# Kernel tuning notes

Hardware: AMD Instinct MI355X
Metric: run time of the kernel (lower is better)

Reference implementation:

```python
import jax, jax.numpy as jnp
import numpy as np

A = 32          # num input capsule types
PSIZE = 16      # caps_size (pose matrix 4x4)
MD = 4          # mat_dim = sqrt(caps_size)
NCLS = 10       # output capsules / classes
KF = 5          # routing kernel (final_shape)
KK = KF * KF
KKA = KK * A
ITERS = 3
FINAL_LAMBDA = 0.01
EPS = 1e-12
LN2PI = float(np.log(2.0 * np.pi))
BN_EPS = 1e-5


def unfold(x, k, stride, pad):
    # torch.nn.functional.unfold: [b,C,h,w] -> [b, C*k*k, L], (c, kh, kw) channel-major
    b, c, h, w = x.shape
    if pad:
        x = jnp.pad(x, ((0, 0), (0, 0), (pad, pad), (pad, pad)))
    oh = (h + 2 * pad - k) // stride + 1
    ow = (w + 2 * pad - k) // stride + 1
    cols = jnp.stack([
        jnp.stack([x[:, :, i:i + stride * oh:stride, j:j + stride * ow:stride]
                   for j in range(k)], axis=3)
        for i in range(k)], axis=2)          # [b, c, k, k, oh, ow]
    return cols.reshape(b, c * k * k, oh * ow)


def conv3x3(x, w):
    return jax.lax.conv_general_dilated(x, w, (1, 1), [(1, 1), (1, 1)],
                                        dimension_numbers=('NCHW', 'OIHW', 'NCHW'))


def bn_inf(x, g, b, m, v):
    scale = g / jnp.sqrt(v + BN_EPS)
    return (x - m[None, :, None, None]) * scale[None, :, None, None] + b[None, :, None, None]


def em_routing(a_in, pose, W, beta_u, beta_a):
    b = a_in.shape[0]
    # pose votes
    pu = unfold(pose, KF, 1, 0)                     # [b, A*PSIZE*KK, l]
    l = pu.shape[-1]
    pu = pu.reshape(b, A, PSIZE, KK, l).transpose(0, 4, 3, 1, 2).reshape(b, l, KKA, PSIZE)
    pm = pu.reshape(b, l, KKA, MD, MD)[:, :, :, None]        # [b,l,kkA,1,md,md]
    v = jnp.matmul(pm, W)                                    # [b,l,kkA,B,md,md]
    v = v.reshape(b, l, KKA, NCLS, PSIZE)
    # activations
    au = unfold(a_in, KF, 1, 0).reshape(b, A, KK, l).transpose(0, 3, 2, 1).reshape(b, l, KKA)
    r = jnp.ones((b, l, KKA, NCLS, 1), v.dtype)
    a_out = mu = None
    for i in range(ITERS):
        lam = FINAL_LAMBDA * (1.0 - 0.95 ** (i + 1))
        # M-step
        rw = r * au[:, :, :, None, None]
        r_sum = rw.sum(axis=2, keepdims=True)                # [b,l,1,B,1]
        coeff = rw / (r_sum + EPS)
        mu = (coeff * v).sum(axis=2, keepdims=True)          # [b,l,1,B,psize]
        sigma_sq = (coeff * (v - mu) ** 2).sum(axis=2, keepdims=True) + EPS
        r_s = r_sum[:, :, 0]                                 # [b,l,B,1]
        sig = sigma_sq[:, :, 0]                              # [b,l,B,psize]
        cost_h = (beta_u + 0.5 * jnp.log(sig)) * r_s         # log(sqrt(s)) = 0.5*log(s)
        a_out = jax.nn.sigmoid(lam * (beta_a - cost_h.sum(axis=3)))   # [b,l,B]
        if i < ITERS - 1:
            # E-step (note: log(sigma_sq * ln2pi) as in original code)
            ln_p = (-0.5 * jnp.sum(jnp.log(sigma_sq * LN2PI), axis=-1)
                    - jnp.sum((v - mu) ** 2 / (2.0 * sigma_sq), axis=-1))   # [b,l,kkA,B]
            ln_ap = ln_p + jnp.log(a_out)[:, :, None, :]
            r = jax.nn.softmax(ln_ap, axis=-1)[..., None]
    oh = int(np.floor(np.sqrt(l)))
    pose_out = mu[:, :, 0].reshape(b, l, -1).transpose(0, 2, 1).reshape(b, -1, oh, oh)
    a_map = a_out.transpose(0, 2, 1).reshape(b, -1, oh, oh)
    return a_map, pose_out


def setup_inputs():
    key = jax.random.key(0)
    ks = jax.random.split(key, 14)
    batch = 256
    x = jax.random.normal(ks[0], (batch, 512, 5, 5), jnp.float32)
    w_a = jax.random.normal(ks[1], (A, 512, 3, 3), jnp.float32) * 0.02
    w_pose = jax.random.normal(ks[2], (A * PSIZE, 512, 3, 3), jnp.float32) * 0.02
    bn_a_g = 1.0 + 0.1 * jax.random.normal(ks[3], (A,), jnp.float32)
    bn_a_b = 0.1 * jax.random.normal(ks[4], (A,), jnp.float32)
    bn_a_m = 0.1 * jax.random.normal(ks[5], (A,), jnp.float32)
    bn_a_v = jax.random.uniform(ks[6], (A,), jnp.float32, 0.5, 1.5)
    C2 = A * PSIZE
    bn_p_g = 1.0 + 0.1 * jax.random.normal(ks[7], (C2,), jnp.float32)
    bn_p_b = 0.1 * jax.random.normal(ks[8], (C2,), jnp.float32)
    bn_p_m = 0.1 * jax.random.normal(ks[9], (C2,), jnp.float32)
    bn_p_v = jax.random.uniform(ks[10], (C2,), jnp.float32, 0.5, 1.5)
    W = jax.random.normal(ks[11], (KKA, NCLS, MD, MD), jnp.float32) * 0.25
    beta_u = jnp.zeros((1, 1, NCLS, 1), jnp.float32)
    beta_a = jnp.zeros((1, 1, NCLS), jnp.float32)
    return {"x": x, "w_a": w_a, "w_pose": w_pose,
            "bn_a_g": bn_a_g, "bn_a_b": bn_a_b, "bn_a_m": bn_a_m, "bn_a_v": bn_a_v,
            "bn_p_g": bn_p_g, "bn_p_b": bn_p_b, "bn_p_m": bn_p_m, "bn_p_v": bn_p_v,
            "W": W, "beta_u": beta_u, "beta_a": beta_a}


def reference(x, w_a, w_pose, bn_a_g, bn_a_b, bn_a_m, bn_a_v,
              bn_p_g, bn_p_b, bn_p_m, bn_p_v, W, beta_u, beta_a):
    a = jax.nn.sigmoid(bn_inf(conv3x3(x, w_a), bn_a_g, bn_a_b, bn_a_m, bn_a_v))
    pose = bn_inf(conv3x3(x, w_pose), bn_p_g, bn_p_b, bn_p_m, bn_p_v)
    a_map, _ = em_routing(a, pose, W, beta_u, beta_a)
    out = a_map.reshape(a_map.shape[0], -1)          # [b, 10]
    out = out / out.sum(axis=1, keepdims=True)
    return jnp.log(out)
```

## Files before the change

kernel.cpp:

```cpp
#include <hip/hip_runtime.h>
#include <math.h>

#define CIN 512
#define NCLS 10
#define KDIM 4608
#define NTOT 6400
#define MPAD 640
#define BK 128
#define NKT 36
#define NABLK (5 * NKT)
#define LN2PI_F 1.8378770664093453f

typedef __attribute__((ext_vector_type(8))) short bf16x8;
typedef __attribute__((ext_vector_type(4))) float f32x4;

typedef const __attribute__((address_space(1))) void* gas_ptr;
typedef __attribute__((address_space(3))) void* las_ptr;

__device__ __forceinline__ void async_copy16(const void* g, void* l) {
    __builtin_amdgcn_global_load_lds((gas_ptr)g, (las_ptr)l, 16, 0, 0);
}

__device__ __forceinline__ unsigned short f2bf(float f) {
    unsigned int u = __float_as_uint(f);
    u = (u + 0x7fffu + ((u >> 16) & 1u)) >> 16;
    return (unsigned short)u;
}
__device__ __forceinline__ float bf2f(unsigned short s) {
    return __uint_as_float(((unsigned int)s) << 16);
}
__device__ __forceinline__ float fexp(float x) { return __expf(x); }
__device__ __forceinline__ float flog(float x) { return __logf(x); }

__global__ __launch_bounds__(1024) void pack_kernel(
    const float* __restrict__ x,
    const float* __restrict__ w_pose, const float* __restrict__ w_a,
    const float* __restrict__ bn_p_g, const float* __restrict__ bn_p_b,
    const float* __restrict__ bn_p_m, const float* __restrict__ bn_p_v,
    const float* __restrict__ bn_a_g, const float* __restrict__ bn_a_b,
    const float* __restrict__ bn_a_m, const float* __restrict__ bn_a_v,
    const float* __restrict__ Wm,
    unsigned short* __restrict__ At, unsigned short* __restrict__ Wmb,
    float* __restrict__ sc, float* __restrict__ bi,
    unsigned short* __restrict__ Bt)
{
    __shared__ __align__(16) float xs[CIN * 25];
    const int bid = blockIdx.x;
    const int t = threadIdx.x;

    if (bid < 256) {
        const int b = bid;
        const float4* xb = reinterpret_cast<const float4*>(x + (size_t)b * (CIN * 25));
        for (int f4 = t; f4 < (CIN * 25) / 4; f4 += 1024)
            reinterpret_cast<float4*>(xs)[f4] = xb[f4];
        __syncthreads();

        for (int w = t; w < 25 * (KDIM / 8); w += 1024) {
            const int ch = w / 25;
            const int px = w - ch * 25;
            const int py = px / 5, qx = px % 5;
            const int k0 = ch * 8;
            unsigned short v[8];
            #pragma unroll
            for (int j = 0; j < 8; ++j) {
                const int k = k0 + j;
                const int ci = k / 9;
                const int kk = k - ci * 9;
                const int dy = kk / 3, dx = kk - dy * 3;
                const int yy = py + dy - 1, xx = qx + dx - 1;
                const bool ok = (yy >= 0) & (yy < 5) & (xx >= 0) & (xx < 5);
                v[j] = ok ? f2bf(xs[ci * 25 + yy * 5 + xx]) : (unsigned short)0;
            }
            int4 o;
            o.x = (int)v[0] | ((int)v[1] << 16);
            o.y = (int)v[2] | ((int)v[3] << 16);
            o.z = (int)v[4] | ((int)v[5] << 16);
            o.w = (int)v[6] | ((int)v[7] << 16);
            const int n = b * 25 + px;
            const int nblk = n >> 7, nr = n & 127;
            const int kt = k0 >> 7;
            const int kc8 = (k0 >> 3) & 15;
            const int c = kc8 * 128 + (nr ^ (kc8 << 2));
            reinterpret_cast<int4*>(Bt + ((((size_t)(nblk * NKT + kt)) << 11) + c) * 8)[0] = o;
        }
        return;
    }

    const int f = (bid - 256) * 1024 + t;
    const int vblk = f >> 8, vt = f & 255;
    if (vblk >= NABLK + 63) return;

    if (vblk >= NABLK) {
        const int chunk = (vblk - NABLK) * 256 + vt;
        if (chunk < 16000) {
            const int e = chunk >> 1, half = chunk & 1;
            const int m = e / 10, c = e - m * 10;
            const int kk = m >> 5, a = m & 31;
            const int de = (kk * 10 + c) * 32 + a;
            const float4* s4 = reinterpret_cast<const float4*>(Wm + (size_t)chunk * 8);
            float4 x0 = s4[0], x1 = s4[1];
            int4 o;
            o.x = (int)f2bf(x0.x) | ((int)f2bf(x0.y) << 16);
            o.y = (int)f2bf(x0.z) | ((int)f2bf(x0.w) << 16);
            o.z = (int)f2bf(x1.x) | ((int)f2bf(x1.y) << 16);
            o.w = (int)f2bf(x1.z) | ((int)f2bf(x1.w) << 16);
            reinterpret_cast<int4*>(Wmb + ((size_t)de * 2 + half) * 8)[0] = o;
        }
        return;
    }

    const int mblk = vblk / NKT;
    if (vblk == 0) {
        for (int i = vt; i < MPAD; i += 256) {
            float s = 0.f, b = 0.f;
            if (i < 512) {
                s = bn_p_g[i] / sqrtf(bn_p_v[i] + 1e-5f);
                b = bn_p_b[i] - bn_p_m[i] * s;
            } else if (i < 544) {
                const int j = i - 512;
                s = bn_a_g[j] / sqrtf(bn_a_v[j] + 1e-5f);
                b = bn_a_b[j] - bn_a_m[j] * s;
            }
            sc[i] = s; bi[i] = b;
        }
    }

    const int kt = vblk - mblk * NKT;
    #pragma unroll
    for (int j = 0; j < 8; ++j) {
        const int c = vt + j * 256;
        const int kc8 = c >> 7, slot = c & 127;
        const int row = mblk * 128 + (slot ^ (kc8 << 2));
        const int k0 = (kt * 16 + kc8) * 8;
        float v[8] = {0.f,0.f,0.f,0.f,0.f,0.f,0.f,0.f};
        if (row < 512) {
            const float4* s4 = reinterpret_cast<const float4*>(w_pose + (size_t)row * KDIM + k0);
            float4 x0 = s4[0], x1 = s4[1];
            v[0]=x0.x; v[1]=x0.y; v[2]=x0.z; v[3]=x0.w;
            v[4]=x1.x; v[5]=x1.y; v[6]=x1.z; v[7]=x1.w;
        } else if (row < 544) {
            const float4* s4 = reinterpret_cast<const float4*>(w_a + (size_t)(row - 512) * KDIM + k0);
            float4 x0 = s4[0], x1 = s4[1];
            v[0]=x0.x; v[1]=x0.y; v[2]=x0.z; v[3]=x0.w;
            v[4]=x1.x; v[5]=x1.y; v[6]=x1.z; v[7]=x1.w;
        }
        int4 o;
        o.x = (int)f2bf(v[0]) | ((int)f2bf(v[1]) << 16);
        o.y = (int)f2bf(v[2]) | ((int)f2bf(v[3]) << 16);
        o.z = (int)f2bf(v[4]) | ((int)f2bf(v[5]) << 16);
        o.w = (int)f2bf(v[6]) | ((int)f2bf(v[7]) << 16);
        reinterpret_cast<int4*>(At + ((((size_t)vblk) << 11) + c) * 8)[0] = o;
    }
}

__global__ __launch_bounds__(1024) void gemm_kernel(
    const unsigned short* __restrict__ At,
    const unsigned short* __restrict__ Bt,
    const float* __restrict__ sc, const float* __restrict__ bi,
    unsigned short* __restrict__ Cp,
    float* __restrict__ Ca)
{
    __shared__ __align__(16) unsigned char smem[131072];
    const int t = threadIdx.x;
    const int L = blockIdx.x;
    int mblk, nblk;
    if (L >= 240) { const int i = L - 240; mblk = i >> 1; nblk = 48 + (i & 1); }
    else          { const int q = L / 40, r = L - q * 40;
                    mblk = r >> 3; nblk = q * 8 + (r & 7); }
    const int m0 = mblk * 128, n0 = nblk * 128;
    const int lane = t & 63, w = t >> 6;
    const int g = w >> 2, wq = w & 3;
    const int wm = wq >> 1, wn = wq & 1;
    const int row16 = lane & 15, quad = lane >> 4;

    f32x4 acc[4][4] = {};

    const unsigned short* gAbase = At + (((size_t)mblk * NKT) << 14);
    const unsigned short* gBbase = Bt + (((size_t)nblk * NKT) << 14);

    #define STAGE(kt, s)                                                      \
    {                                                                         \
        unsigned short* As_ = (unsigned short*)(smem + (s) * 65536);          \
        unsigned short* Bs_ = As_ + 16384;                                    \
        const unsigned short* ga = gAbase + ((size_t)(kt) << 14);             \
        const unsigned short* gb = gBbase + ((size_t)(kt) << 14);             \
        _Pragma("unroll")                                                     \
        for (int j = 0; j < 2; ++j) {                                         \
            async_copy16(ga + ((size_t)(j * 1024 + t) << 3),                  \
                         As_ + ((size_t)(j * 1024 + w * 64) << 3));           \
            async_copy16(gb + ((size_t)(j * 1024 + t) << 3),                  \
                         Bs_ + ((size_t)(j * 1024 + w * 64) << 3));           \
        }                                                                     \
    }

    #define COMPUTE(s)                                                        \
    {                                                                         \
        const unsigned short* As_ = (const unsigned short*)(smem + (s) * 65536);\
        const unsigned short* Bs_ = As_ + 16384;                              \
        const int kc8b = g * 4 + quad;                                        \
        const int sw = kc8b << 2;                                             \
        bf16x8 af[4], bfr[4];                                                 \
        _Pragma("unroll")                                                     \
        for (int mt = 0; mt < 4; ++mt)                                        \
            af[mt] = *reinterpret_cast<const bf16x8*>(                        \
                &As_[(size_t)(kc8b * 128 + ((wm * 64 + mt * 16 + row16) ^ sw)) * 8]);\
        _Pragma("unroll")                                                     \
        for (int nt = 0; nt < 4; ++nt)                                        \
            bfr[nt] = *reinterpret_cast<const bf16x8*>(                       \
                &Bs_[(size_t)(kc8b * 128 + ((wn * 64 + nt * 16 + row16) ^ sw)) * 8]);\
        _Pragma("unroll")                                                     \
        for (int mt = 0; mt < 4; ++mt)                                        \
            _Pragma("unroll")                                                 \
            for (int nt = 0; nt < 4; ++nt)                                    \
                acc[mt][nt] = __builtin_amdgcn_mfma_f32_16x16x32_bf16(        \
                    af[mt], bfr[nt], acc[mt][nt], 0, 0, 0);                   \
    }

    STAGE(0, 0);
    for (int kt = 0; kt < NKT; ++kt) {
        __syncthreads();
        if (kt + 1 < NKT) STAGE(kt + 1, (kt + 1) & 1);
        COMPUTE(kt & 1);
    }
    #undef STAGE
    #undef COMPUTE

    f32x4* mb = (f32x4*)smem;
    #pragma unroll
    for (int r = 1; r < 4; ++r) {
        __syncthreads();
        if (g == r) {
            f32x4* dst = mb + wq * 1024;
            #pragma unroll
            for (int i = 0; i < 16; ++i)
                dst[i * 64 + lane] = acc[i >> 2][i & 3];
        }
        __syncthreads();
        if (g == 0) {
            const f32x4* src = mb + wq * 1024;
            #pragma unroll
            for (int i = 0; i < 16; ++i)
                acc[i >> 2][i & 3] += src[i * 64 + lane];
        }
    }

    if (g == 0) {
        #pragma unroll
        for (int mt = 0; mt < 4; ++mt) {
            const int mbase = m0 + wm * 64 + mt * 16 + quad * 4;
            if (mbase >= 544) continue;
            #pragma unroll
            for (int rg = 0; rg < 4; ++rg) {
                const int m = mbase + rg;
                const float s = sc[m], bbx = bi[m];
                #pragma unroll
                for (int nt = 0; nt < 4; ++nt) {
                    const int n = n0 + wn * 64 + nt * 16 + row16;
                    const float v = fmaf(acc[mt][nt][rg], s, bbx);
                    if (m < 512) Cp[(size_t)m * NTOT + n] = f2bf(v);
                    else Ca[(size_t)(m - 512) * NTOT + n] = 1.f / (1.f + fexp(-v));
                }
            }
        }
    }
}

__global__ __launch_bounds__(640, 1) void em_kernel(
    const unsigned short* __restrict__ Cp,
    const float* __restrict__ Ca,
    const unsigned short* __restrict__ Wmb,
    const float* __restrict__ beta_u, const float* __restrict__ beta_a,
    float* __restrict__ out)
{
    __shared__ __align__(16) unsigned short psh[25][2][32][8];
    __shared__ __align__(16) unsigned short wsh[2 * 20480];
    __shared__ float aush[800];
    __shared__ float lnq[NCLS][800];
    __shared__ float mu_sh[NCLS][16];
    __shared__ float i2s_sh[NCLS][16];
    __shared__ float costp[2][NCLS];
    __shared__ float slgp[2][NCLS];
    __shared__ float Kc_sh[NCLS];
    __shared__ float aout_sh[NCLS];

    const int b = blockIdx.x, t = threadIdx.x;
    const int c = t >> 6;
    const int rh = (t >> 5) & 1;
    const int a = t & 31;

    const int gu = t ^ ((t >> 3) & 3);
    const int r2 = (c * 32 + a) * 2;
    const int u0 = r2 ^ ((r2 >> 3) & 3);

    #define STAGEW(qq, ss)                                                   \
    {                                                                        \
        const int nkk_ = ((qq) == 6) ? 1 : 4;                                \
        const unsigned short* gW = Wmb + (size_t)(qq) * 4 * 5120;            \
        unsigned short* lW = wsh + (size_t)(ss) * 20480;                     \
        for (int kki = 0; kki < nkk_; ++kki)                                 \
            async_copy16(gW + (size_t)(kki * 640 + gu) * 8,                  \
                         lW + (size_t)(kki * 640 + t) * 8);                  \
    }

    const unsigned short* pb = Cp + (size_t)b * 25;
    for (int f = t; f < 12800; f += 640) {
        const int c2 = f / 25, px = f - c2 * 25;
        const int e = c2 & 15;
        psh[px][e >> 3][c2 >> 4][e & 7] = pb[(size_t)c2 * NTOT + px];
    }
    const float* ab = Ca + (size_t)b * 25;
    for (int f = t; f < 800; f += 640) {
        const int ci = f / 25, px = f - ci * 25;
        aush[px * 32 + ci] = ab[(size_t)ci * NTOT + px];
    }
    __syncthreads();

    const float bu = beta_u[c], ba = beta_a[c];
    float muL[8], i2sL[8], KcL = 0.f;

    #define VOTE(w0_, w1_, p_, vv)                                           \
        {                                                                    \
            float pm[8], wv[16];                                             \
            const unsigned int pu[4] = {(unsigned)p_.x, (unsigned)p_.y,      \
                                        (unsigned)p_.z, (unsigned)p_.w};     \
            _Pragma("unroll")                                                \
            for (int i = 0; i < 4; ++i) {                                    \
                pm[2*i]   = __uint_as_float(pu[i] << 16);                    \
                pm[2*i+1] = __uint_as_float(pu[i] & 0xFFFF0000u);            \
            }                                                                \
            const unsigned int uu[8] = {(unsigned)w0_.x,(unsigned)w0_.y,     \
                (unsigned)w0_.z,(unsigned)w0_.w,(unsigned)w1_.x,             \
                (unsigned)w1_.y,(unsigned)w1_.z,(unsigned)w1_.w};            \
            _Pragma("unroll")                                                \
            for (int i = 0; i < 8; ++i) {                                    \
                wv[2*i]   = __uint_as_float(uu[i] << 16);                    \
                wv[2*i+1] = __uint_as_float(uu[i] & 0xFFFF0000u);            \
            }                                                                \
            _Pragma("unroll")                                                \
            for (int jr = 0; jr < 2; ++jr) {                                 \
                _Pragma("unroll")                                            \
                for (int s = 0; s < 4; ++s) {                                \
                    float av = 0.f;                                          \
                    _Pragma("unroll")                                        \
                    for (int tt = 0; tt < 4; ++tt)                           \
                        av = fmaf(pm[jr*4+tt], wv[tt*4+s], av);              \
                    vv[jr*4+s] = av;                                         \
                }                                                            \
            }                                                                \
        }

    float p95 = 1.f;
    for (int it = 0; it < 3; ++it) {
        p95 *= 0.95f;
        const float lam = 0.01f * (1.f - p95);

        if (it > 0) {
            STAGEW(0, 0);
            __syncthreads();
            for (int qc = 0; qc < 7; ++qc) {
                if (qc < 6) STAGEW(qc + 1, (qc + 1) & 1);
                const unsigned short* wb = wsh + (size_t)(qc & 1) * 20480;
                #pragma unroll
                for (int kkin = 0; kkin < 4; ++kkin) {
                    const int kk = qc * 4 + kkin;
                    if (kk < 25) {
                        const unsigned short* wrow = wb + kkin * 5120;
                        const int4 w0 = *reinterpret_cast<const int4*>(wrow + (size_t)u0 * 8);
                        const int4 w1 = *reinterpret_cast<const int4*>(wrow + (size_t)(u0 ^ 1) * 8);
                        const int4 p = *reinterpret_cast<const int4*>(&psh[kk][rh][a][0]);
                        float vv[8];
                        VOTE(w0, w1, p, vv);
                        float qacc = (rh == 0) ? KcL : 0.f;
                        #pragma unroll
                        for (int j = 0; j < 8; ++j) {
                            const float d = vv[j] - muL[j];
                            qacc -= d * d * i2sL[j];
                        }
                        qacc += __shfl_xor(qacc, 32);
                        if (rh == 0) lnq[c][kk * 32 + a] = qacc;
                    }
                }
                __syncthreads();
            }
            for (int m = t; m < 800; m += 640) {
                float qv[NCLS];
                #pragma unroll
                for (int cc = 0; cc < NCLS; ++cc) qv[cc] = lnq[cc][m];
                float mx = qv[0];
                #pragma unroll
                for (int cc = 1; cc < NCLS; ++cc) mx = fmaxf(mx, qv[cc]);
                float ev[NCLS];
                float den = 0.f;
                #pragma unroll
                for (int cc = 0; cc < NCLS; ++cc) {
                    ev[cc] = fexp(qv[cc] - mx);
                    den += ev[cc];
                }
                const float s = aush[m] * __builtin_amdgcn_rcpf(den);
                #pragma unroll
                for (int cc = 0; cc < NCLS; ++cc)
                    lnq[cc][m] = ev[cc] * s;
            }
            __syncthreads();
        }

        float S0 = 0.f, S1[8], S2[8];
        #pragma unroll
        for (int j = 0; j < 8; ++j) { S1[j] = 0.f; S2[j] = 0.f; }

        STAGEW(0, 0);
        __syncthreads();
        for (int qc = 0; qc < 7; ++qc) {
            if (qc < 6) STAGEW(qc + 1, (qc + 1) & 1);
            const unsigned short* wb = wsh + (size_t)(qc & 1) * 20480;
            #pragma unroll
            for (int kkin = 0; kkin < 4; ++kkin) {
                const int kk = qc * 4 + kkin;
                if (kk < 25) {
                    const unsigned short* wrow = wb + kkin * 5120;
                    const int4 w0 = *reinterpret_cast<const int4*>(wrow + (size_t)u0 * 8);
                    const int4 w1 = *reinterpret_cast<const int4*>(wrow + (size_t)(u0 ^ 1) * 8);
                    const int4 p = *reinterpret_cast<const int4*>(&psh[kk][rh][a][0]);
                    float vv[8];
                    VOTE(w0, w1, p, vv);
                    const int m = kk * 32 + a;
                    const float rw = (it == 0) ? aush[m] : lnq[c][m];
                    S0 += rw;
                    #pragma unroll
                    for (int j = 0; j < 8; ++j) {
                        const float rv = rw * vv[j];
                        S1[j] += rv;
                        S2[j] = fmaf(rv, vv[j], S2[j]);
                    }
                }
            }
            __syncthreads();
        }

        #pragma unroll
        for (int off = 16; off >= 1; off >>= 1) {
            S0 += __shfl_xor(S0, off);
            #pragma unroll
            for (int j = 0; j < 8; ++j) {
                S1[j] += __shfl_xor(S1[j], off);
                S2[j] += __shfl_xor(S2[j], off);
            }
        }

        if (a == 0) {
            const float s0e = S0 + 1e-12f;
            const float inv = 1.f / s0e;
            float cost_ = 0.f, slg_ = 0.f;
            #pragma unroll
            for (int j = 0; j < 8; ++j) {
                const float mu_ = S1[j] * inv;
                const float sg = (S2[j] - 2.f * mu_ * S1[j] + mu_ * mu_ * S0) * inv
                                 + 1e-12f;
                cost_ += bu + 0.5f * flog(sg);
                slg_ += flog(sg * LN2PI_F);
                mu_sh[c][rh * 8 + j] = mu_;
                i2s_sh[c][rh * 8 + j] = 0.5f / sg;
            }
            costp[rh][c] = cost_;
            slgp[rh][c] = slg_;
        }
        __syncthreads();
        if (a == 0 && rh == 0) {
            const float costsum = (costp[0][c] + costp[1][c]) * S0;
            const float aout = 1.f / (1.f + fexp(-(lam * (ba - costsum))));
            aout_sh[c] = aout;
            Kc_sh[c] = flog(aout) - 0.5f * (slgp[0][c] + slgp[1][c]);
        }
        __syncthreads();
        if (it < 2) {
            #pragma unroll
            for (int j = 0; j < 8; ++j) {
                muL[j] = mu_sh[c][rh * 8 + j];
                i2sL[j] = i2s_sh[c][rh * 8 + j];
            }
            KcL = Kc_sh[c];
        }
    }

    if (t < NCLS) {
        float s = 0.f;
        #pragma unroll
        for (int cc = 0; cc < NCLS; ++cc) s += aout_sh[cc];
        out[b * NCLS + t] = flog(aout_sh[t] / s);
    }
    #undef VOTE
    #undef STAGEW
}

extern "C" void kernel_launch(void* const* d_in, const int* in_sizes, int n_in,
                              void* d_out, int out_size, void* d_ws, size_t ws_size,
                              hipStream_t stream) {
    const float* x      = (const float*)d_in[0];
    const float* w_a    = (const float*)d_in[1];
    const float* w_pose = (const float*)d_in[2];
    const float* bn_a_g = (const float*)d_in[3];
    const float* bn_a_b = (const float*)d_in[4];
    const float* bn_a_m = (const float*)d_in[5];
    const float* bn_a_v = (const float*)d_in[6];
    const float* bn_p_g = (const float*)d_in[7];
    const float* bn_p_b = (const float*)d_in[8];
    const float* bn_p_m = (const float*)d_in[9];
    const float* bn_p_v = (const float*)d_in[10];
    const float* Wm     = (const float*)d_in[11];
    const float* beta_u = (const float*)d_in[12];
    const float* beta_a = (const float*)d_in[13];
    float* out = (float*)d_out;

    char* p = (char*)d_ws;
    unsigned short* At  = (unsigned short*)p;  p += (size_t)MPAD * KDIM * 2;
    unsigned short* Bt  = (unsigned short*)p;  p += (size_t)NTOT * KDIM * 2;
    unsigned short* Wmb = (unsigned short*)p;  p += (size_t)800 * NCLS * 16 * 2;
    unsigned short* Cp  = (unsigned short*)p;  p += (size_t)512 * NTOT * 2;
    float* Ca = (float*)p;                     p += (size_t)32 * NTOT * 4;
    float* sc = (float*)p;                     p += MPAD * 4;
    float* bi = (float*)p;                     p += MPAD * 4;

    pack_kernel<<<317, 1024, 0, stream>>>(x, w_pose, w_a,
                                          bn_p_g, bn_p_b, bn_p_m, bn_p_v,
                                          bn_a_g, bn_a_b, bn_a_m, bn_a_v,
                                          Wm, At, Wmb, sc, bi, Bt);
    gemm_kernel<<<250, 1024, 0, stream>>>(At, Bt, sc, bi, Cp, Ca);
    em_kernel<<<256, 640, 0, stream>>>(Cp, Ca, Wmb, beta_u, beta_a, out);
}
```

Baseline: 230.9 us.

## Load routing weights directly from global into registers, drop LDS staging

The EM routing kernel no longer double-buffers the transformation weights W through shared memory with async copies and per-chunk barriers. Each thread now reads its own 32-byte weight slice straight from global memory into registers, prefetching one step ahead. The 25 kernel positions are split into two interleaved streams (0-12 and 13-24) with separate accumulators to raise instruction-level parallelism. This removes seven block-wide syncs per pass and frees 80 KB of LDS, but relies on L2/cache hits for the repeated per-block weight reads and uses more registers.

New measurement: 233.1 us. No clear change (+1.0%).

```diff
diff --git a/kernel.cpp b/kernel.cpp
--- a/kernel.cpp
+++ b/kernel.cpp
@@ -273,7 +273,6 @@
     float* __restrict__ out)
 {
     __shared__ __align__(16) unsigned short psh[25][2][32][8];
-    __shared__ __align__(16) unsigned short wsh[2 * 20480];
     __shared__ float aush[800];
     __shared__ float lnq[NCLS][800];
     __shared__ float mu_sh[NCLS][16];
@@ -288,20 +287,6 @@
     const int rh = (t >> 5) & 1;
     const int a = t & 31;
 
-    const int gu = t ^ ((t >> 3) & 3);
-    const int r2 = (c * 32 + a) * 2;
-    const int u0 = r2 ^ ((r2 >> 3) & 3);
-
-    #define STAGEW(qq, ss)                                                   \
-    {                                                                        \
-        const int nkk_ = ((qq) == 6) ? 1 : 4;                                \
-        const unsigned short* gW = Wmb + (size_t)(qq) * 4 * 5120;            \
-        unsigned short* lW = wsh + (size_t)(ss) * 20480;                     \
-        for (int kki = 0; kki < nkk_; ++kki)                                 \
-            async_copy16(gW + (size_t)(kki * 640 + gu) * 8,                  \
-                         lW + (size_t)(kki * 640 + t) * 8);                  \
-    }
-
     const unsigned short* pb = Cp + (size_t)b * 25;
     for (int f = t; f < 12800; f += 640) {
         const int c2 = f / 25, px = f - c2 * 25;
@@ -317,6 +302,8 @@
 
     const float bu = beta_u[c], ba = beta_a[c];
     float muL[8], i2sL[8], KcL = 0.f;
+    const unsigned short* wbase  = Wmb + ((size_t)(c * 32 + a)) * 16;
+    const unsigned short* wbaseB = wbase + (size_t)13 * 5120;
 
     #define VOTE(w0_, w1_, p_, vv)                                           \
         {                                                                    \
@@ -355,33 +342,53 @@
         const float lam = 0.01f * (1.f - p95);
 
         if (it > 0) {
-            STAGEW(0, 0);
+            int4 wA0 = *reinterpret_cast<const int4*>(wbase);
+            int4 wA1 = *reinterpret_cast<const int4*>(wbase + 8);
+            int4 wB0 = *reinterpret_cast<const int4*>(wbaseB);
+            int4 wB1 = *reinterpret_cast<const int4*>(wbaseB + 8);
+            int4 pA = *reinterpret_cast<const int4*>(&psh[0][rh][a][0]);
+            int4 pB = *reinterpret_cast<const int4*>(&psh[13][rh][a][0]);
+            for (int kh = 0; kh < 13; ++kh) {
+                const int4 a0 = wA0, a1 = wA1, p0 = pA;
+                const int4 b0 = wB0, b1 = wB1, p1 = pB;
+                if (kh < 12) {
+                    const unsigned short* wnA = wbase + (size_t)(kh + 1) * 5120;
+                    wA0 = *reinterpret_cast<const int4*>(wnA);
+                    wA1 = *reinterpret_cast<const int4*>(wnA + 8);
+                    pA  = *reinterpret_cast<const int4*>(&psh[kh + 1][rh][a][0]);
+                    if (kh < 11) {
+                        const unsigned short* wnB = wbaseB + (size_t)(kh + 1) * 5120;
+                        wB0 = *reinterpret_cast<const int4*>(wnB);
+                        wB1 = *reinterpret_cast<const int4*>(wnB + 8);
+                        pB  = *reinterpret_cast<const int4*>(&psh[kh + 14][rh][a][0]);
+                    }
+                }
+                float vvA[8];
+                VOTE(a0, a1, p0, vvA);
+                float qA = (rh == 0) ? KcL : 0.f;
+                #pragma unroll
+                for (int j = 0; j < 8; ++j) {
+                    const float d = vvA[j] - muL[j];
+                    qA -= d * d * i2sL[j];
+                }
+                float qB = (rh == 0) ? KcL : 0.f;
+                if (kh < 12) {
+                    float vvB[8];
+                    VOTE(b0, b1, p1, vvB);
+                    #pragma unroll
+                    for (int j = 0; j < 8; ++j) {
+                        const float d = vvB[j] - muL[j];
+                        qB -= d * d * i2sL[j];
+                    }
+                }
+                qA += __shfl_xor(qA, 32);
+                qB += __shfl_xor(qB, 32);
+                if (rh == 0) {
+                    lnq[c][kh * 32 + a] = qA;
+                    if (kh < 12) lnq[c][(kh + 13) * 32 + a] = qB;
+                }
+            }
             __syncthreads();
-            for (int qc = 0; qc < 7; ++qc) {
-                if (qc < 6) STAGEW(qc + 1, (qc + 1) & 1);
-                const unsigned short* wb = wsh + (size_t)(qc & 1) * 20480;
-                #pragma unroll
-                for (int kkin = 0; kkin < 4; ++kkin) {
-                    const int kk = qc * 4 + kkin;
-                    if (kk < 25) {
-                        const unsigned short* wrow = wb + kkin * 5120;
-                        const int4 w0 = *reinterpret_cast<const int4*>(wrow + (size_t)u0 * 8);
-                        const int4 w1 = *reinterpret_cast<const int4*>(wrow + (size_t)(u0 ^ 1) * 8);
-                        const int4 p = *reinterpret_cast<const int4*>(&psh[kk][rh][a][0]);
-                        float vv[8];
-                        VOTE(w0, w1, p, vv);
-                        float qacc = (rh == 0) ? KcL : 0.f;
-                        #pragma unroll
-                        for (int j = 0; j < 8; ++j) {
-                            const float d = vv[j] - muL[j];
-                            qacc -= d * d * i2sL[j];
-                        }
-                        qacc += __shfl_xor(qacc, 32);
-                        if (rh == 0) lnq[c][kk * 32 + a] = qacc;
-                    }
-                }
-                __syncthreads();
-            }
             for (int m = t; m < 800; m += 640) {
                 float qv[NCLS];
                 #pragma unroll
@@ -404,39 +411,65 @@
             __syncthreads();
         }
 
-        float S0 = 0.f, S1[8], S2[8];
+        float S0a = 0.f, S1a[8], S2a[8];
+        float S0b = 0.f, S1b[8], S2b[8];
         #pragma unroll
-        for (int j = 0; j < 8; ++j) { S1[j] = 0.f; S2[j] = 0.f; }
-
-        STAGEW(0, 0);
-        __syncthreads();
-        for (int qc = 0; qc < 7; ++qc) {
-            if (qc < 6) STAGEW(qc + 1, (qc + 1) & 1);
-            const unsigned short* wb = wsh + (size_t)(qc & 1) * 20480;
-            #pragma unroll
-            for (int kkin = 0; kkin < 4; ++kkin) {
-                const int kk = qc * 4 + kkin;
-                if (kk < 25) {
-                    const unsigned short* wrow = wb + kkin * 5120;
-                    const int4 w0 = *reinterpret_cast<const int4*>(wrow + (size_t)u0 * 8);
-                    const int4 w1 = *reinterpret_cast<const int4*>(wrow + (size_t)(u0 ^ 1) * 8);
-                    const int4 p = *reinterpret_cast<const int4*>(&psh[kk][rh][a][0]);
-                    float vv[8];
-                    VOTE(w0, w1, p, vv);
-                    const int m = kk * 32 + a;
-                    const float rw = (it == 0) ? aush[m] : lnq[c][m];
-                    S0 += rw;
-                    #pragma unroll
-                    for (int j = 0; j < 8; ++j) {
-                        const float rv = rw * vv[j];
-                        S1[j] += rv;
-                        S2[j] = fmaf(rv, vv[j], S2[j]);
-                    }
-                }
-            }
-            __syncthreads();
-        }
-
+        for (int j = 0; j < 8; ++j) { S1a[j] = 0.f; S2a[j] = 0.f;
+                                      S1b[j] = 0.f; S2b[j] = 0.f; }
+
+        int4 wA0 = *reinterpret_cast<const int4*>(wbase);
+        int4 wA1 = *reinterpret_cast<const int4*>(wbase + 8);
+        int4 wB0 = *reinterpret_cast<const int4*>(wbaseB);
+        int4 wB1 = *reinterpret_cast<const int4*>(wbaseB + 8);
+        int4 pA = *reinterpret_cast<const int4*>(&psh[0][rh][a][0]);
+        int4 pB = *reinterpret_cast<const int4*>(&psh[13][rh][a][0]);
+        for (int kh = 0; kh < 13; ++kh) {
+            const int4 a0 = wA0, a1 = wA1, p0 = pA;
+            const int4 b0 = wB0, b1 = wB1, p1 = pB;
+            if (kh < 12) {
+                const unsigned short* wnA = wbase + (size_t)(kh + 1) * 5120;
+                wA0 = *reinterpret_cast<const int4*>(wnA);
+                wA1 = *reinterpret_cast<const int4*>(wnA + 8);
+                pA  = *reinterpret_cast<const int4*>(&psh[kh + 1][rh][a][0]);
+                if (kh < 11) {
+                    const unsigned short* wnB = wbaseB + (size_t)(kh + 1) * 5120;
+                    wB0 = *reinterpret_cast<const int4*>(wnB);
+                    wB1 = *reinterpret_cast<const int4*>(wnB + 8);
+                    pB  = *reinterpret_cast<const int4*>(&psh[kh + 14][rh][a][0]);
+                }
+            }
+            {
+                float vvA[8];
+                VOTE(a0, a1, p0, vvA);
+                const int m = kh * 32 + a;
+                const float rw = (it == 0) ? aush[m] : lnq[c][m];
+                S0a += rw;
+                #pragma unroll
+                for (int j = 0; j < 8; ++j) {
+                    const float rv = rw * vvA[j];
+                    S1a[j] += rv;
+                    S2a[j] = fmaf(rv, vvA[j], S2a[j]);
+                }
+            }
+            if (kh < 12) {
+                float vvB[8];
+                VOTE(b0, b1, p1, vvB);
+                const int m = (kh + 13) * 32 + a;
+                const float rw = (it == 0) ? aush[m] : lnq[c][m];
+                S0b += rw;
+                #pragma unroll
+                for (int j = 0; j < 8; ++j) {
+                    const float rv = rw * vvB[j];
+                    S1b[j] += rv;
+                    S2b[j] = fmaf(rv, vvB[j], S2b[j]);
+                }
+            }
+        }
+
+        float S0 = S0a + S0b, S1[8], S2[8];
+        #pragma unroll
+        for (int j = 0; j < 8; ++j) { S1[j] = S1a[j] + S1b[j];
+                                      S2[j] = S2a[j] + S2b[j]; }
         #pragma unroll
         for (int off = 16; off >= 1; off >>= 1) {
             S0 += __shfl_xor(S0, off);
@@ -489,7 +522,6 @@
         out[b * NCLS + t] = flog(aout_sh[t] / s);
     }
     #undef VOTE
-    #undef STAGEW
 }
 
 extern "C" void kernel_launch(void* const* d_in, const int* in_sizes, int n_in,
```

## Read fp32 routing weights directly from global with register prefetch instead of LDS staging

Applied to the files above, without the earlier changes.

The EM routing kernel no longer stages bf16 transform weights into double-buffered shared memory with async copies and per-chunk barriers. Each thread now loads its own fp32 weight rows straight from global memory (L2-resident, shared across the 256 blocks) with one- or two-step register prefetch. This removes the barriers and the bf16 unpacking inside the vote loops and raises weight precision to fp32. In exchange it doubles weight bytes and relies on cache hits for the repeated per-block reads.

After: 405.2 us. 1.75x slower.

```diff
diff --git a/kernel.cpp b/kernel.cpp
--- a/kernel.cpp
+++ b/kernel.cpp
@@ -40,7 +40,7 @@
     const float* __restrict__ bn_a_g, const float* __restrict__ bn_a_b,
     const float* __restrict__ bn_a_m, const float* __restrict__ bn_a_v,
     const float* __restrict__ Wm,
-    unsigned short* __restrict__ At, unsigned short* __restrict__ Wmb,
+    unsigned short* __restrict__ At, float* __restrict__ Wmbf,
     float* __restrict__ sc, float* __restrict__ bi,
     unsigned short* __restrict__ Bt)
 {
@@ -98,13 +98,9 @@
             const int kk = m >> 5, a = m & 31;
             const int de = (kk * 10 + c) * 32 + a;
             const float4* s4 = reinterpret_cast<const float4*>(Wm + (size_t)chunk * 8);
-            float4 x0 = s4[0], x1 = s4[1];
-            int4 o;
-            o.x = (int)f2bf(x0.x) | ((int)f2bf(x0.y) << 16);
-            o.y = (int)f2bf(x0.z) | ((int)f2bf(x0.w) << 16);
-            o.z = (int)f2bf(x1.x) | ((int)f2bf(x1.y) << 16);
-            o.w = (int)f2bf(x1.z) | ((int)f2bf(x1.w) << 16);
-            reinterpret_cast<int4*>(Wmb + ((size_t)de * 2 + half) * 8)[0] = o;
+            float4* d4 = reinterpret_cast<float4*>(Wmbf + ((size_t)de * 2 + half) * 8);
+            d4[0] = s4[0];
+            d4[1] = s4[1];
         }
         return;
     }
@@ -268,12 +264,11 @@
 __global__ __launch_bounds__(640, 1) void em_kernel(
     const unsigned short* __restrict__ Cp,
     const float* __restrict__ Ca,
-    const unsigned short* __restrict__ Wmb,
+    const float* __restrict__ Wmbf,
     const float* __restrict__ beta_u, const float* __restrict__ beta_a,
     float* __restrict__ out)
 {
     __shared__ __align__(16) unsigned short psh[25][2][32][8];
-    __shared__ __align__(16) unsigned short wsh[2 * 20480];
     __shared__ float aush[800];
     __shared__ float lnq[NCLS][800];
     __shared__ float mu_sh[NCLS][16];
@@ -288,20 +283,6 @@
     const int rh = (t >> 5) & 1;
     const int a = t & 31;
 
-    const int gu = t ^ ((t >> 3) & 3);
-    const int r2 = (c * 32 + a) * 2;
-    const int u0 = r2 ^ ((r2 >> 3) & 3);
-
-    #define STAGEW(qq, ss)                                                   \
-    {                                                                        \
-        const int nkk_ = ((qq) == 6) ? 1 : 4;                                \
-        const unsigned short* gW = Wmb + (size_t)(qq) * 4 * 5120;            \
-        unsigned short* lW = wsh + (size_t)(ss) * 20480;                     \
-        for (int kki = 0; kki < nkk_; ++kki)                                 \
-            async_copy16(gW + (size_t)(kki * 640 + gu) * 8,                  \
-                         lW + (size_t)(kki * 640 + t) * 8);                  \
-    }
-
     const unsigned short* pb = Cp + (size_t)b * 25;
     for (int f = t; f < 12800; f += 640) {
         const int c2 = f / 25, px = f - c2 * 25;
@@ -317,10 +298,11 @@
 
     const float bu = beta_u[c], ba = beta_a[c];
     float muL[8], i2sL[8], KcL = 0.f;
-
-    #define VOTE(w0_, w1_, p_, vv)                                           \
+    const float* wbase = Wmbf + ((size_t)(c * 32 + a)) * 16;
+
+    #define VOTE(w0_, w1_, w2_, w3_, p_, vv)                                 \
         {                                                                    \
-            float pm[8], wv[16];                                             \
+            float pm[8];                                                     \
             const unsigned int pu[4] = {(unsigned)p_.x, (unsigned)p_.y,      \
                                         (unsigned)p_.z, (unsigned)p_.w};     \
             _Pragma("unroll")                                                \
@@ -328,14 +310,10 @@
                 pm[2*i]   = __uint_as_float(pu[i] << 16);                    \
                 pm[2*i+1] = __uint_as_float(pu[i] & 0xFFFF0000u);            \
             }                                                                \
-            const unsigned int uu[8] = {(unsigned)w0_.x,(unsigned)w0_.y,     \
-                (unsigned)w0_.z,(unsigned)w0_.w,(unsigned)w1_.x,             \
-                (unsigned)w1_.y,(unsigned)w1_.z,(unsigned)w1_.w};            \
-            _Pragma("unroll")                                                \
-            for (int i = 0; i < 8; ++i) {                                    \
-                wv[2*i]   = __uint_as_float(uu[i] << 16);                    \
-                wv[2*i+1] = __uint_as_float(uu[i] & 0xFFFF0000u);            \
-            }                                                                \
+            const float wv[16] = {w0_.x, w0_.y, w0_.z, w0_.w,                \
+                                  w1_.x, w1_.y, w1_.z, w1_.w,                \
+                                  w2_.x, w2_.y, w2_.z, w2_.w,                \
+                                  w3_.x, w3_.y, w3_.z, w3_.w};               \
             _Pragma("unroll")                                                \
             for (int jr = 0; jr < 2; ++jr) {                                 \
                 _Pragma("unroll")                                            \
@@ -355,33 +333,30 @@
         const float lam = 0.01f * (1.f - p95);
 
         if (it > 0) {
-            STAGEW(0, 0);
+            const float4* wp = reinterpret_cast<const float4*>(wbase);
+            float4 r0 = wp[0], r1 = wp[1], r2 = wp[2], r3 = wp[3];
+            int4 pr = *reinterpret_cast<const int4*>(&psh[0][rh][a][0]);
+            for (int kk = 0; kk < 25; ++kk) {
+                const float4 w0 = r0, w1 = r1, w2 = r2, w3 = r3;
+                const int4 p = pr;
+                if (kk < 24) {
+                    const float4* wn = reinterpret_cast<const float4*>(
+                        wbase + (size_t)(kk + 1) * 5120);
+                    r0 = wn[0]; r1 = wn[1]; r2 = wn[2]; r3 = wn[3];
+                    pr = *reinterpret_cast<const int4*>(&psh[kk + 1][rh][a][0]);
+                }
+                float vv[8];
+                VOTE(w0, w1, w2, w3, p, vv);
+                float q = (rh == 0) ? KcL : 0.f;
+                #pragma unroll
+                for (int j = 0; j < 8; ++j) {
+                    const float d = vv[j] - muL[j];
+                    q -= d * d * i2sL[j];
+                }
+                q += __shfl_xor(q, 32);
+                if (rh == 0) lnq[c][kk * 32 + a] = q;
+            }
             __syncthreads();
-            for (int qc = 0; qc < 7; ++qc) {
-                if (qc < 6) STAGEW(qc + 1, (qc + 1) & 1);
-                const unsigned short* wb = wsh + (size_t)(qc & 1) * 20480;
-                #pragma unroll
-                for (int kkin = 0; kkin < 4; ++kkin) {
-                    const int kk = qc * 4 + kkin;
-                    if (kk < 25) {
-                        const unsigned short* wrow = wb + kkin * 5120;
-                        const int4 w0 = *reinterpret_cast<const int4*>(wrow + (size_t)u0 * 8);
-                        const int4 w1 = *reinterpret_cast<const int4*>(wrow + (size_t)(u0 ^ 1) * 8);
-                        const int4 p = *reinterpret_cast<const int4*>(&psh[kk][rh][a][0]);
-                        float vv[8];
-                        VOTE(w0, w1, p, vv);
-                        float qacc = (rh == 0) ? KcL : 0.f;
-                        #pragma unroll
-                        for (int j = 0; j < 8; ++j) {
-                            const float d = vv[j] - muL[j];
-                            qacc -= d * d * i2sL[j];
-                        }
-                        qacc += __shfl_xor(qacc, 32);
-                        if (rh == 0) lnq[c][kk * 32 + a] = qacc;
-                    }
-                }
-                __syncthreads();
-            }
             for (int m = t; m < 800; m += 640) {
                 float qv[NCLS];
                 #pragma unroll
@@ -408,33 +383,33 @@
         #pragma unroll
         for (int j = 0; j < 8; ++j) { S1[j] = 0.f; S2[j] = 0.f; }
 
-        STAGEW(0, 0);
-        __syncthreads();
-        for (int qc = 0; qc < 7; ++qc) {
-            if (qc < 6) STAGEW(qc + 1, (qc + 1) & 1);
-            const unsigned short* wb = wsh + (size_t)(qc & 1) * 20480;
-            #pragma unroll
-            for (int kkin = 0; kkin < 4; ++kkin) {
-                const int kk = qc * 4 + kkin;
-                if (kk < 25) {
-                    const unsigned short* wrow = wb + kkin * 5120;
-                    const int4 w0 = *reinterpret_cast<const int4*>(wrow + (size_t)u0 * 8);
-                    const int4 w1 = *reinterpret_cast<const int4*>(wrow + (size_t)(u0 ^ 1) * 8);
-                    const int4 p = *reinterpret_cast<const int4*>(&psh[kk][rh][a][0]);
-                    float vv[8];
-                    VOTE(w0, w1, p, vv);
-                    const int m = kk * 32 + a;
-                    const float rw = (it == 0) ? aush[m] : lnq[c][m];
-                    S0 += rw;
-                    #pragma unroll
-                    for (int j = 0; j < 8; ++j) {
-                        const float rv = rw * vv[j];
-                        S1[j] += rv;
-                        S2[j] = fmaf(rv, vv[j], S2[j]);
-                    }
-                }
-            }
-            __syncthreads();
+        const float4* wpA = reinterpret_cast<const float4*>(wbase);
+        const float4* wpB = reinterpret_cast<const float4*>(wbase + 5120);
+        float4 a0 = wpA[0], a1 = wpA[1], a2 = wpA[2], a3 = wpA[3];
+        float4 b0 = wpB[0], b1 = wpB[1], b2 = wpB[2], b3 = wpB[3];
+        int4 pr = *reinterpret_cast<const int4*>(&psh[0][rh][a][0]);
+        for (int kk = 0; kk < 25; ++kk) {
+            const float4 w0 = a0, w1 = a1, w2 = a2, w3 = a3;
+            const int4 p = pr;
+            a0 = b0; a1 = b1; a2 = b2; a3 = b3;
+            if (kk < 23) {
+                const float4* wn = reinterpret_cast<const float4*>(
+                    wbase + (size_t)(kk + 2) * 5120);
+                b0 = wn[0]; b1 = wn[1]; b2 = wn[2]; b3 = wn[3];
+            }
+            if (kk < 24)
+                pr = *reinterpret_cast<const int4*>(&psh[kk + 1][rh][a][0]);
+            float vv[8];
+            VOTE(w0, w1, w2, w3, p, vv);
+            const int m = kk * 32 + a;
+            const float rw = (it == 0) ? aush[m] : lnq[c][m];
+            S0 += rw;
+            #pragma unroll
+            for (int j = 0; j < 8; ++j) {
+                const float rv = rw * vv[j];
+                S1[j] += rv;
+                S2[j] = fmaf(rv, vv[j], S2[j]);
+            }
         }
 
         #pragma unroll
@@ -489,7 +464,6 @@
         out[b * NCLS + t] = flog(aout_sh[t] / s);
     }
     #undef VOTE
-    #undef STAGEW
 }
 
 extern "C" void kernel_launch(void* const* d_in, const int* in_sizes, int n_in,
@@ -514,7 +488,7 @@
     char* p = (char*)d_ws;
     unsigned short* At  = (unsigned short*)p;  p += (size_t)MPAD * KDIM * 2;
     unsigned short* Bt  = (unsigned short*)p;  p += (size_t)NTOT * KDIM * 2;
-    unsigned short* Wmb = (unsigned short*)p;  p += (size_t)800 * NCLS * 16 * 2;
+    float* Wmbf = (float*)p;                   p += (size_t)800 * NCLS * 16 * 4;
     unsigned short* Cp  = (unsigned short*)p;  p += (size_t)512 * NTOT * 2;
     float* Ca = (float*)p;                     p += (size_t)32 * NTOT * 4;
     float* sc = (float*)p;                     p += MPAD * 4;
@@ -523,7 +497,7 @@
     pack_kernel<<<317, 1024, 0, stream>>>(x, w_pose, w_a,
                                           bn_p_g, bn_p_b, bn_p_m, bn_p_v,
                                           bn_a_g, bn_a_b, bn_a_m, bn_a_v,
-                                          Wm, At, Wmb, sc, bi, Bt);
+                                          Wm, At, Wmbf, sc, bi, Bt);
     gemm_kernel<<<250, 1024, 0, stream>>>(At, Bt, sc, bi, Cp, Ca);
-    em_kernel<<<256, 640, 0, stream>>>(Cp, Ca, Wmb, beta_u, beta_a, out);
-}
+    em_kernel<<<256, 640, 0, stream>>>(Cp, Ca, Wmbf, beta_u, beta_a, out);
+}
```
